# Kernel tuning notes

Measured on AMD Instinct MI355X. Metric: run time of the kernel, lower is better.

## Reference

```python
import jax, jax.numpy as jnp
import numpy as np

N = 100000   # nodes
E = 1600000  # edges (avg degree 16)
IN, HID, OUT, HEADS = 8, 32, 16, 4


def setup_inputs() -> dict:
    key = jax.random.key(0)
    ks = jax.random.split(key, 12)
    def g(k, shape, fan):
        return (jax.random.normal(k, shape, jnp.float32) / np.float32(np.sqrt(fan)))
    x = jax.random.normal(ks[0], (N, IN), jnp.float32)
    edge_index = jax.random.randint(ks[1], (2, E), 0, N, dtype=jnp.int64)
    return {
        "x": x,
        "edge_index": edge_index,
        "W1": g(ks[2], (IN, HEADS * HID), IN),
        "att_src1": g(ks[3], (HEADS, HID), HID),
        "att_dst1": g(ks[4], (HEADS, HID), HID),
        "b1": jnp.zeros((HEADS * HID,), jnp.float32),
        "W2": g(ks[5], (HEADS * HID, OUT), HEADS * HID),
        "att_src2": g(ks[6], (1, OUT), OUT),
        "att_dst2": g(ks[7], (1, OUT), OUT),
        "b2": jnp.zeros((OUT,), jnp.float32),
        "Wc1": g(ks[8], (OUT, 8), OUT),
        "bc1": jnp.zeros((8,), jnp.float32),
        "Wc2": g(ks[9], (8, 1), 8),
        "bc2": jnp.zeros((1,), jnp.float32),
    }


def _gat_layer(x, W, att_src, att_dst, bias, src, dst, n, concat):
    """PyG GATConv (eval mode): gather -> per-edge attention -> segment softmax -> scatter."""
    H, D = att_src.shape
    h = (x @ W).reshape(n, H, D)                       # [N,H,D]
    a_s = jnp.einsum("nhd,hd->nh", h, att_src)          # [N,H]
    a_d = jnp.einsum("nhd,hd->nh", h, att_dst)          # [N,H]
    e = jax.nn.leaky_relu(a_s[src] + a_d[dst], 0.2)     # [Etot,H]
    m = jax.ops.segment_max(e, dst, num_segments=n)     # per-dst max for stable softmax
    m = jnp.where(jnp.isfinite(m), m, 0.0)
    e = jnp.exp(e - m[dst])
    denom = jax.ops.segment_sum(e, dst, num_segments=n)
    alpha = e / (denom[dst] + 1e-16)                    # [Etot,H]
    out = jax.ops.segment_sum(h[src] * alpha[:, :, None], dst, num_segments=n)  # [N,H,D]
    out = out.reshape(n, H * D) if concat else out.mean(axis=1)
    return out + bias


def reference(x, edge_index, W1, att_src1, att_dst1, b1, W2, att_src2, att_dst2, b2, Wc1, bc1, Wc2, bc2):
    n = x.shape[0]
    loops = jnp.arange(n, dtype=edge_index.dtype)       # add_self_loops=True (PyG default)
    src = jnp.concatenate([edge_index[0], loops])
    dst = jnp.concatenate([edge_index[1], loops])
    h = jax.nn.elu(_gat_layer(x, W1, att_src1, att_dst1, b1, src, dst, n, concat=True))
    emb = jax.nn.elu(_gat_layer(h, W2, att_src2, att_dst2, b2, src, dst, n, concat=False))
    risk = jax.nn.sigmoid(jax.nn.relu(emb @ Wc1 + bc1) @ Wc2 + bc2)
    return emb, risk
```

## Files before the change

kernel.cpp:

```cpp
#include <hip/hip_runtime.h>
#include <hip/hip_fp16.h>
#include <math.h>

#define N_NODES 100000
#define N_EDGES 1600000
#define F_IN 8
#define HID 32
#define HEADS 4
#define F1 128
#define F2 16
#define NB 391
#define NBLK_BIN 391
#define NBLK_A 391
#define BCAP 4864

__device__ __forceinline__ float leaky(float x){ return x > 0.f ? x : 0.2f * x; }
__device__ __forceinline__ float elu1(float x){ return x > 0.f ? x : __expf(x) - 1.f; }

__global__ __launch_bounds__(256) void k_bin_attn(
    const int* __restrict__ src, const int* __restrict__ dst,
    int* __restrict__ bucketCnt, unsigned int* __restrict__ ebuf,
    const float* __restrict__ x, const float* __restrict__ W1,
    const float* __restrict__ as1w, const float* __restrict__ ad1w,
    float* __restrict__ xa){
    __shared__ float smem[1344];
    int t = threadIdx.x;
    if (blockIdx.x < NBLK_BIN){
        int* hist    = (int*)smem;
        int* basePos = hist + NB;
        int* cur     = basePos + NB;
        for (int j = t; j < NB; j += 256) hist[j] = 0;
        __syncthreads();
        int base = blockIdx.x * 4096;
        int dv[16];
        #pragma unroll
        for (int j = 0; j < 16; j++){
            int e = base + j * 256 + t;
            dv[j] = (e < N_EDGES) ? dst[e] : -1;
            if (dv[j] >= 0) atomicAdd(&hist[dv[j] >> 8], 1);
        }
        __syncthreads();
        for (int j = t; j < NB; j += 256){
            int h = hist[j];
            if (h) basePos[j] = atomicAdd(&bucketCnt[j], h);
            cur[j] = 0;
        }
        __syncthreads();
        #pragma unroll
        for (int j = 0; j < 16; j++){
            if (dv[j] >= 0){
                int e = base + j * 256 + t;
                int d = dv[j];
                int b = d >> 8;
                int off = atomicAdd(&cur[b], 1);
                ebuf[b * BCAP + basePos[b] + off] = ((unsigned)(d & 255) << 17) | (unsigned)src[e];
            }
        }
    } else {
        float* W1s  = smem;
        float* atts = smem + 1024;
        float* attd = smem + 1152;
        float* cs   = smem + 1280;
        float* cd   = smem + 1312;
        ((float4*)W1s)[t] = ((const float4*)W1)[t];
        if (t < 128){ atts[t] = as1w[t]; attd[t] = ad1w[t]; }
        __syncthreads();
        if (t < 64){
            int m = t & 7, h = (t >> 3) & 3;
            bool sel = t >= 32;
            const float* wrow = W1s + m * F1 + h * 32;
            const float* av   = (sel ? attd : atts) + h * 32;
            float s = 0.f;
            #pragma unroll
            for (int d = 0; d < 32; d++) s += wrow[d] * av[d];
            (sel ? cd : cs)[h * 8 + m] = s;
        }
        __syncthreads();
        int n = (blockIdx.x - NBLK_BIN) * 256 + t;
        if (n < N_NODES){
            float4 x0 = ((const float4*)x)[n * 2];
            float4 x1 = ((const float4*)x)[n * 2 + 1];
            float4 osv, odv;
            float* po = (float*)&osv;
            float* pd = (float*)&odv;
            #pragma unroll
            for (int h = 0; h < 4; h++){
                const float* c0 = cs + h * 8;
                const float* c1 = cd + h * 8;
                po[h] = x0.x*c0[0] + x0.y*c0[1] + x0.z*c0[2] + x0.w*c0[3]
                      + x1.x*c0[4] + x1.y*c0[5] + x1.z*c0[6] + x1.w*c0[7];
                pd[h] = x0.x*c1[0] + x0.y*c1[1] + x0.z*c1[2] + x0.w*c1[3]
                      + x1.x*c1[4] + x1.y*c1[5] + x1.z*c1[6] + x1.w*c1[7];
            }
            float* px = xa + (size_t)n * 16;
            *(float4*)(px)      = x0;
            *(float4*)(px + 4)  = x1;
            *(float4*)(px + 8)  = osv;
            *(float4*)(px + 12) = odv;
        }
    }
}

__global__ __launch_bounds__(256) void k_local_csr(
    const int* __restrict__ bucketCnt, const unsigned int* __restrict__ ebuf,
    int* __restrict__ row_ptr, int* __restrict__ esrc){
    __shared__ int deg[256];
    __shared__ int scn[256];
    __shared__ int cntAll[NB];
    __shared__ unsigned int segs[BCAP];
    int b = blockIdx.x, t = threadIdx.x;
    deg[t] = 0;
    for (int j = t; j < NB; j += 256) cntAll[j] = bucketCnt[j];
    __syncthreads();
    int partial = 0;
    for (int j = t; j < b; j += 256) partial += cntAll[j];
    scn[t] = partial;
    __syncthreads();
    for (int off = 128; off > 0; off >>= 1){
        if (t < off) scn[t] += scn[t + off];
        __syncthreads();
    }
    int sbase = scn[0];
    int cnt = cntAll[b];
    __syncthreads();
    const unsigned int* seg = ebuf + b * BCAP;
    for (int i = t; i < cnt; i += 256){
        unsigned int e = seg[i];
        segs[i] = e;
        atomicAdd(&deg[e >> 17], 1);
    }
    __syncthreads();
    int v = deg[t];
    scn[t] = v;
    __syncthreads();
    for (int off = 1; off < 256; off <<= 1){
        int xx = (t >= off) ? scn[t - off] : 0;
        __syncthreads();
        scn[t] += xx;
        __syncthreads();
    }
    int excl = scn[t] - v;
    int start = sbase + excl;
    int n = b * 256 + t;
    if (n < N_NODES) row_ptr[n] = start;
    if (b == NB - 1 && t == 0) row_ptr[N_NODES] = sbase + cnt;
    deg[t] = start;
    __syncthreads();
    for (int i = t; i < cnt; i += 256){
        unsigned int e = segs[i];
        int pos = atomicAdd(&deg[e >> 17], 1);
        esrc[pos] = (int)(e & 0x1FFFFu);
    }
}

__global__ __launch_bounds__(256) void k_agg1(
    const float* __restrict__ xa, const int* __restrict__ row_ptr, const int* __restrict__ esrc,
    float* __restrict__ xagg, float* __restrict__ dden){
    int t = threadIdx.x;
    int wv = t >> 6, lane = t & 63;
    int n = blockIdx.x * 4 + wv;
    int g = lane >> 4;
    int l = lane & 15;
    int hd = l >> 2;
    int c2 = (l & 3) * 2;

    float vn = xa[(size_t)n * 16 + l];
    float adh = __shfl(vn, 12 + hd, 16);

    float den = 0.f, ac0 = 0.f, ac1 = 0.f;
    if (g == 0){
        float w = __expf(leaky(__shfl(vn, 8 + hd, 16) + adh));
        den = w;
        ac0 = w * __shfl(vn, c2, 16);
        ac1 = w * __shfl(vn, c2 + 1, 16);
    }
    int start = row_ptr[n], end = row_ptr[n + 1];
    int len = end - start;
    int chunk = (len + 3) >> 2;
    int i = start + g * chunk;
    int e = i + chunk; if (e > end) e = end;
    for (; i + 3 < e; i += 4){
        int s0 = esrc[i], s1 = esrc[i + 1], s2 = esrc[i + 2], s3 = esrc[i + 3];
        float v0 = xa[(size_t)s0 * 16 + l];
        float v1 = xa[(size_t)s1 * 16 + l];
        float v2 = xa[(size_t)s2 * 16 + l];
        float v3 = xa[(size_t)s3 * 16 + l];
        float w0 = __expf(leaky(__shfl(v0, 8 + hd, 16) + adh));
        float w1 = __expf(leaky(__shfl(v1, 8 + hd, 16) + adh));
        float w2 = __expf(leaky(__shfl(v2, 8 + hd, 16) + adh));
        float w3 = __expf(leaky(__shfl(v3, 8 + hd, 16) + adh));
        den += (w0 + w1) + (w2 + w3);
        ac0 = fmaf(w0, __shfl(v0, c2, 16), ac0); ac1 = fmaf(w0, __shfl(v0, c2 + 1, 16), ac1);
        ac0 = fmaf(w1, __shfl(v1, c2, 16), ac0); ac1 = fmaf(w1, __shfl(v1, c2 + 1, 16), ac1);
        ac0 = fmaf(w2, __shfl(v2, c2, 16), ac0); ac1 = fmaf(w2, __shfl(v2, c2 + 1, 16), ac1);
        ac0 = fmaf(w3, __shfl(v3, c2, 16), ac0); ac1 = fmaf(w3, __shfl(v3, c2 + 1, 16), ac1);
    }
    for (; i < e; i++){
        int s0 = esrc[i];
        float v0 = xa[(size_t)s0 * 16 + l];
        float w0 = __expf(leaky(__shfl(v0, 8 + hd, 16) + adh));
        den += w0;
        ac0 = fmaf(w0, __shfl(v0, c2, 16), ac0); ac1 = fmaf(w0, __shfl(v0, c2 + 1, 16), ac1);
    }
    den += __shfl_xor(den, 16); den += __shfl_xor(den, 32);
    ac0 += __shfl_xor(ac0, 16); ac0 += __shfl_xor(ac0, 32);
    ac1 += __shfl_xor(ac1, 16); ac1 += __shfl_xor(ac1, 32);

    if (lane < 16){
        float2 o; o.x = ac0; o.y = ac1;
        *(float2*)(xagg + (size_t)n * 32 + 2 * l) = o;
        if ((l & 3) == 0) dden[(size_t)n * 4 + hd] = den;
    }
}

__global__ __launch_bounds__(256) void k_epi(
    const float* __restrict__ xagg, const float* __restrict__ dden,
    const float* __restrict__ W1, const float* __restrict__ W2,
    const float* __restrict__ b1, const float* __restrict__ as2w, const float* __restrict__ ad2w,
    __half* __restrict__ h2h, float* __restrict__ a_s2, float* __restrict__ a_d2){
    __shared__ __half2 W1h[F_IN * 64];
    __shared__ __half2 W2t[F2 * 64];
    __shared__ __half2 hlsh[16 * 68];
    int t = threadIdx.x;
    {
        float4 w1v = ((const float4*)W1)[t];
        int m = t >> 5, j = (2 * t) & 63;
        W1h[m * 64 + j]     = __floats2half2_rn(w1v.x, w1v.y);
        W1h[m * 64 + j + 1] = __floats2half2_rn(w1v.z, w1v.w);
        #pragma unroll
        for (int hf = 0; hf < 2; hf++){
            int p = t + hf * 256;
            float4 wv = ((const float4*)W2)[p];
            int k = p >> 2, dbase = (p & 3) * 4;
            float vals[4] = {wv.x, wv.y, wv.z, wv.w};
            #pragma unroll
            for (int c = 0; c < 4; c++){
                int dw = (dbase + c) * 64 + (k >> 1);
                int sdw = dw ^ (((dw >> 6) & 7) << 2);
                ((__half*)W2t)[2 * sdw + (k & 1)] = __float2half(vals[c]);
            }
        }
    }
    __syncthreads();

    int nn = t >> 4, q = t & 15;
    int n = blockIdx.x * 16 + nn;
    int hd = q >> 2;

    const float* xg = xagg + (size_t)n * 32 + hd * 8;
    float4 xga = *(const float4*)(xg);
    float4 xgb = *(const float4*)(xg + 4);
    float invd = 1.f / dden[(size_t)n * 4 + hd];
    float xv[8] = {xga.x, xga.y, xga.z, xga.w, xgb.x, xgb.y, xgb.z, xgb.w};
    float pre[8] = {0,0,0,0,0,0,0,0};
    #pragma unroll
    for (int m = 0; m < 8; m++){
        float4 raw = *(const float4*)(W1h + m * 64 + 4 * q);
        const __half2* wp = (const __half2*)&raw;
        float xm = xv[m];
        float2 f0 = __half22float2(wp[0]);
        float2 f1 = __half22float2(wp[1]);
        float2 f2 = __half22float2(wp[2]);
        float2 f3 = __half22float2(wp[3]);
        pre[0] = fmaf(xm, f0.x, pre[0]); pre[1] = fmaf(xm, f0.y, pre[1]);
        pre[2] = fmaf(xm, f1.x, pre[2]); pre[3] = fmaf(xm, f1.y, pre[3]);
        pre[4] = fmaf(xm, f2.x, pre[4]); pre[5] = fmaf(xm, f2.y, pre[5]);
        pre[6] = fmaf(xm, f3.x, pre[6]); pre[7] = fmaf(xm, f3.y, pre[7]);
    }
    float4 ba = *(const float4*)(b1 + 8 * q);
    float4 bb = *(const float4*)(b1 + 8 * q + 4);
    __half2 hout[4];
    hout[0] = __floats2half2_rn(elu1(pre[0] * invd + ba.x), elu1(pre[1] * invd + ba.y));
    hout[1] = __floats2half2_rn(elu1(pre[2] * invd + ba.z), elu1(pre[3] * invd + ba.w));
    hout[2] = __floats2half2_rn(elu1(pre[4] * invd + bb.x), elu1(pre[5] * invd + bb.y));
    hout[3] = __floats2half2_rn(elu1(pre[6] * invd + bb.z), elu1(pre[7] * invd + bb.w));
    *(float4*)(hlsh + nn * 68 + 4 * q) = *(float4*)hout;
    __syncthreads();

    float dot = 0.f;
    #pragma unroll
    for (int ob = 0; ob < 8; ob++){
        __half2 acc2 = __float2half2_rn(0.f);
        #pragma unroll
        for (int kb = ob * 2; kb < ob * 2 + 2; kb++){
            float4 hr = *(const float4*)(hlsh + nn * 68 + 4 * kb);
            int dwb = 64 * q + 4 * kb;
            float4 wr = *(const float4*)(W2t + (dwb ^ (((dwb >> 6) & 7) << 2)));
            const __half2* hp  = (const __half2*)&hr;
            const __half2* wp2 = (const __half2*)&wr;
            acc2 = __hfma2(hp[0], wp2[0], acc2);
            acc2 = __hfma2(hp[1], wp2[1], acc2);
            acc2 = __hfma2(hp[2], wp2[2], acc2);
            acc2 = __hfma2(hp[3], wp2[3], acc2);
        }
        float2 fa = __half22float2(acc2);
        dot += fa.x + fa.y;
    }
    float ps = dot * as2w[q];
    float pd = dot * ad2w[q];
    #pragma unroll
    for (int off = 8; off >= 1; off >>= 1){
        ps += __shfl_down(ps, off, 16);
        pd += __shfl_down(pd, off, 16);
    }
    if (q == 0){ a_s2[n] = ps; a_d2[n] = pd; }
    h2h[(size_t)n * F2 + q] = __float2half(dot);
}

__global__ __launch_bounds__(256) void k_agg2(
    const __half* __restrict__ h2h, const float* __restrict__ a_s2, const float* __restrict__ a_d2,
    const int* __restrict__ row_ptr, const int* __restrict__ esrc,
    const float* __restrict__ b2, const float* __restrict__ Wc1, const float* __restrict__ bc1,
    const float* __restrict__ Wc2, const float* __restrict__ bc2, float* __restrict__ out){
    int t = threadIdx.x;
    int wv = t >> 6, lane = t & 63;
    int n = blockIdx.x * 4 + wv;
    int g = lane >> 3;
    int l = lane & 7;
    float adn = a_d2[n];
    const __half* hb2 = h2h + 2 * l;

    float den = 0.f, acc0 = 0.f, acc1 = 0.f;
    if (g == 0){
        float w = __expf(leaky(a_s2[n] + adn));
        den = w;
        float2 f = __half22float2(*(const __half2*)(hb2 + ((unsigned)n << 4)));
        acc0 = w * f.x; acc1 = w * f.y;
    }
    int start = row_ptr[n], end = row_ptr[n + 1];
    int len = end - start;
    int chunk = (len + 7) >> 3;
    int i = start + g * chunk;
    int e = i + chunk; if (e > end) e = end;
    for (int base = i; base < e; base += 4){
        bool v1 = base + 1 < e, v2 = base + 2 < e, v3 = base + 3 < e;
        int s0 = esrc[base];
        int s1 = v1 ? esrc[base + 1] : s0;
        int s2 = v2 ? esrc[base + 2] : s0;
        int s3 = v3 ? esrc[base + 3] : s0;
        float a0 = a_s2[s0], a1 = a_s2[s1], a2 = a_s2[s2], a3 = a_s2[s3];
        __half2 p0 = *(const __half2*)(hb2 + ((unsigned)s0 << 4));
        __half2 p1 = *(const __half2*)(hb2 + ((unsigned)s1 << 4));
        __half2 p2 = *(const __half2*)(hb2 + ((unsigned)s2 << 4));
        __half2 p3 = *(const __half2*)(hb2 + ((unsigned)s3 << 4));
        float w0 = __expf(leaky(a0 + adn));
        float w1 = v1 ? __expf(leaky(a1 + adn)) : 0.f;
        float w2 = v2 ? __expf(leaky(a2 + adn)) : 0.f;
        float w3 = v3 ? __expf(leaky(a3 + adn)) : 0.f;
        den += (w0 + w1) + (w2 + w3);
        float2 f0 = __half22float2(p0), f1 = __half22float2(p1);
        float2 f2 = __half22float2(p2), f3 = __half22float2(p3);
        acc0 += w0 * f0.x + w1 * f1.x + w2 * f2.x + w3 * f3.x;
        acc1 += w0 * f0.y + w1 * f1.y + w2 * f2.y + w3 * f3.y;
    }
    #pragma unroll
    for (int off = 8; off <= 32; off <<= 1){
        den  += __shfl_xor(den, off);
        acc0 += __shfl_xor(acc0, off);
        acc1 += __shfl_xor(acc1, off);
    }
    float inv = 1.f / (den + 1e-16f);
    float e0v = elu1(acc0 * inv + b2[2 * l]);
    float e1v = elu1(acc1 * inv + b2[2 * l + 1]);
    if (g == 0){
        float2 ov; ov.x = e0v; ov.y = e1v;
        *(float2*)(out + (size_t)n * 16 + 2 * l) = ov;
    }
    float hid = bc1[l];
    #pragma unroll
    for (int j = 0; j < 8; j++){
        float a = __shfl(e0v, j, 8);
        float b = __shfl(e1v, j, 8);
        hid += a * Wc1[(2 * j) * 8 + l] + b * Wc1[(2 * j + 1) * 8 + l];
    }
    float contrib = fmaxf(hid, 0.f) * Wc2[l];
    contrib += __shfl_xor(contrib, 1);
    contrib += __shfl_xor(contrib, 2);
    contrib += __shfl_xor(contrib, 4);
    if (lane == 0) out[(size_t)N_NODES * 16 + n] = 1.f / (1.f + __expf(-(contrib + bc2[0])));
}

extern "C" void kernel_launch(void* const* d_in, const int* in_sizes, int n_in,
                              void* d_out, int out_size, void* d_ws, size_t ws_size,
                              hipStream_t stream){
    const float* x    = (const float*)d_in[0];
    const int*   ei   = (const int*)d_in[1];
    const float* W1   = (const float*)d_in[2];
    const float* as1w = (const float*)d_in[3];
    const float* ad1w = (const float*)d_in[4];
    const float* b1   = (const float*)d_in[5];
    const float* W2   = (const float*)d_in[6];
    const float* as2w = (const float*)d_in[7];
    const float* ad2w = (const float*)d_in[8];
    const float* b2   = (const float*)d_in[9];
    const float* Wc1  = (const float*)d_in[10];
    const float* bc1  = (const float*)d_in[11];
    const float* Wc2  = (const float*)d_in[12];
    const float* bc2  = (const float*)d_in[13];
    float* out = (float*)d_out;
    const int* src = ei;
    const int* dst = ei + N_EDGES;

    float* ws   = (float*)d_ws;
    float* a_s2 = ws;
    float* a_d2 = a_s2 + N_NODES;
    float* xa   = a_d2 + N_NODES;
    float* xagg = xa + (size_t)N_NODES * 16;
    float* dden = xagg + (size_t)N_NODES * 32;
    __half* h2h = (__half*)(dden + (size_t)N_NODES * 4);
    int* bucketCnt = (int*)(h2h + (size_t)N_NODES * 16);
    int* row_ptr  = bucketCnt + NB;
    int* esrc     = row_ptr + N_NODES + 1;
    unsigned int* ebuf = (unsigned int*)(esrc + N_EDGES);

    hipMemsetAsync(bucketCnt, 0, NB * sizeof(int), stream);
    k_bin_attn<<<NBLK_BIN + NBLK_A, 256, 0, stream>>>(
        src, dst, bucketCnt, ebuf, x, W1, as1w, ad1w, xa);
    k_local_csr<<<NB, 256, 0, stream>>>(bucketCnt, ebuf, row_ptr, esrc);
    k_agg1<<<N_NODES / 4, 256, 0, stream>>>(xa, row_ptr, esrc, xagg, dden);
    k_epi<<<N_NODES / 16, 256, 0, stream>>>(
        xagg, dden, W1, W2, b1, as2w, ad2w, h2h, a_s2, a_d2);
    k_agg2<<<N_NODES / 4, 256, 0, stream>>>(h2h, a_s2, a_d2, row_ptr, esrc, b2, Wc1, bc1, Wc2, bc2, out);
}
```

Measured before the change: 242.1 us.

## Halve edges per bin block, widen CSR blocks, predicate agg1 tail loop

The binning kernel now handles 2048 edges per block over twice as many blocks. The local CSR kernel runs with 512 threads per block, and only the first 256 threads do the per-node scan. The agg1 gather loop drops its scalar remainder loop in favour of a predicated 4-wide body that zeroes out-of-range weights. The aim is more parallelism in the preprocessing stages and better memory-level parallelism on short edge tails, at the cost of extra global atomics on bucket counts and some redundant loads.

```diff
diff --git a/kernel.cpp b/kernel.cpp
--- a/kernel.cpp
+++ b/kernel.cpp
@@ -10,7 +10,8 @@
 #define F1 128
 #define F2 16
 #define NB 391
-#define NBLK_BIN 391
+#define NBLK_BIN 782
+#define EDGES_PER_BIN 2048
 #define NBLK_A 391
 #define BCAP 4864
 
@@ -31,10 +32,10 @@
         int* cur     = basePos + NB;
         for (int j = t; j < NB; j += 256) hist[j] = 0;
         __syncthreads();
-        int base = blockIdx.x * 4096;
-        int dv[16];
+        int base = blockIdx.x * EDGES_PER_BIN;
+        int dv[8];
         #pragma unroll
-        for (int j = 0; j < 16; j++){
+        for (int j = 0; j < 8; j++){
             int e = base + j * 256 + t;
             dv[j] = (e < N_EDGES) ? dst[e] : -1;
             if (dv[j] >= 0) atomicAdd(&hist[dv[j] >> 8], 1);
@@ -47,7 +48,7 @@
         }
         __syncthreads();
         #pragma unroll
-        for (int j = 0; j < 16; j++){
+        for (int j = 0; j < 8; j++){
             if (dv[j] >= 0){
                 int e = base + j * 256 + t;
                 int d = dv[j];
@@ -101,22 +102,22 @@
     }
 }
 
-__global__ __launch_bounds__(256) void k_local_csr(
+__global__ __launch_bounds__(512) void k_local_csr(
     const int* __restrict__ bucketCnt, const unsigned int* __restrict__ ebuf,
     int* __restrict__ row_ptr, int* __restrict__ esrc){
     __shared__ int deg[256];
-    __shared__ int scn[256];
+    __shared__ int scn[512];
     __shared__ int cntAll[NB];
     __shared__ unsigned int segs[BCAP];
     int b = blockIdx.x, t = threadIdx.x;
-    deg[t] = 0;
-    for (int j = t; j < NB; j += 256) cntAll[j] = bucketCnt[j];
+    if (t < 256) deg[t] = 0;
+    for (int j = t; j < NB; j += 512) cntAll[j] = bucketCnt[j];
     __syncthreads();
     int partial = 0;
-    for (int j = t; j < b; j += 256) partial += cntAll[j];
+    for (int j = t; j < b; j += 512) partial += cntAll[j];
     scn[t] = partial;
     __syncthreads();
-    for (int off = 128; off > 0; off >>= 1){
+    for (int off = 256; off > 0; off >>= 1){
         if (t < off) scn[t] += scn[t + off];
         __syncthreads();
     }
@@ -124,29 +125,31 @@
     int cnt = cntAll[b];
     __syncthreads();
     const unsigned int* seg = ebuf + b * BCAP;
-    for (int i = t; i < cnt; i += 256){
+    for (int i = t; i < cnt; i += 512){
         unsigned int e = seg[i];
         segs[i] = e;
         atomicAdd(&deg[e >> 17], 1);
     }
     __syncthreads();
-    int v = deg[t];
-    scn[t] = v;
+    int v = (t < 256) ? deg[t] : 0;
+    if (t < 256) scn[t] = v;
     __syncthreads();
     for (int off = 1; off < 256; off <<= 1){
-        int xx = (t >= off) ? scn[t - off] : 0;
-        __syncthreads();
-        scn[t] += xx;
-        __syncthreads();
-    }
-    int excl = scn[t] - v;
-    int start = sbase + excl;
-    int n = b * 256 + t;
-    if (n < N_NODES) row_ptr[n] = start;
+        int xx = (t < 256 && t >= off) ? scn[t - off] : 0;
+        __syncthreads();
+        if (t < 256) scn[t] += xx;
+        __syncthreads();
+    }
+    if (t < 256){
+        int excl = scn[t] - v;
+        int start = sbase + excl;
+        int n = b * 256 + t;
+        if (n < N_NODES) row_ptr[n] = start;
+        deg[t] = start;
+    }
     if (b == NB - 1 && t == 0) row_ptr[N_NODES] = sbase + cnt;
-    deg[t] = start;
-    __syncthreads();
-    for (int i = t; i < cnt; i += 256){
+    __syncthreads();
+    for (int i = t; i < cnt; i += 512){
         unsigned int e = segs[i];
         int pos = atomicAdd(&deg[e >> 17], 1);
         esrc[pos] = (int)(e & 0x1FFFFu);
@@ -179,28 +182,25 @@
     int chunk = (len + 3) >> 2;
     int i = start + g * chunk;
     int e = i + chunk; if (e > end) e = end;
-    for (; i + 3 < e; i += 4){
-        int s0 = esrc[i], s1 = esrc[i + 1], s2 = esrc[i + 2], s3 = esrc[i + 3];
+    for (int base = i; base < e; base += 4){
+        bool b1v = base + 1 < e, b2v = base + 2 < e, b3v = base + 3 < e;
+        int s0 = esrc[base];
+        int s1 = b1v ? esrc[base + 1] : s0;
+        int s2 = b2v ? esrc[base + 2] : s0;
+        int s3 = b3v ? esrc[base + 3] : s0;
         float v0 = xa[(size_t)s0 * 16 + l];
         float v1 = xa[(size_t)s1 * 16 + l];
         float v2 = xa[(size_t)s2 * 16 + l];
         float v3 = xa[(size_t)s3 * 16 + l];
         float w0 = __expf(leaky(__shfl(v0, 8 + hd, 16) + adh));
-        float w1 = __expf(leaky(__shfl(v1, 8 + hd, 16) + adh));
-        float w2 = __expf(leaky(__shfl(v2, 8 + hd, 16) + adh));
-        float w3 = __expf(leaky(__shfl(v3, 8 + hd, 16) + adh));
+        float w1 = b1v ? __expf(leaky(__shfl(v1, 8 + hd, 16) + adh)) : 0.f;
+        float w2 = b2v ? __expf(leaky(__shfl(v2, 8 + hd, 16) + adh)) : 0.f;
+        float w3 = b3v ? __expf(leaky(__shfl(v3, 8 + hd, 16) + adh)) : 0.f;
         den += (w0 + w1) + (w2 + w3);
         ac0 = fmaf(w0, __shfl(v0, c2, 16), ac0); ac1 = fmaf(w0, __shfl(v0, c2 + 1, 16), ac1);
         ac0 = fmaf(w1, __shfl(v1, c2, 16), ac0); ac1 = fmaf(w1, __shfl(v1, c2 + 1, 16), ac1);
         ac0 = fmaf(w2, __shfl(v2, c2, 16), ac0); ac1 = fmaf(w2, __shfl(v2, c2 + 1, 16), ac1);
         ac0 = fmaf(w3, __shfl(v3, c2, 16), ac0); ac1 = fmaf(w3, __shfl(v3, c2 + 1, 16), ac1);
-    }
-    for (; i < e; i++){
-        int s0 = esrc[i];
-        float v0 = xa[(size_t)s0 * 16 + l];
-        float w0 = __expf(leaky(__shfl(v0, 8 + hd, 16) + adh));
-        den += w0;
-        ac0 = fmaf(w0, __shfl(v0, c2, 16), ac0); ac1 = fmaf(w0, __shfl(v0, c2 + 1, 16), ac1);
     }
     den += __shfl_xor(den, 16); den += __shfl_xor(den, 32);
     ac0 += __shfl_xor(ac0, 16); ac0 += __shfl_xor(ac0, 32);
@@ -416,7 +416,7 @@
     hipMemsetAsync(bucketCnt, 0, NB * sizeof(int), stream);
     k_bin_attn<<<NBLK_BIN + NBLK_A, 256, 0, stream>>>(
         src, dst, bucketCnt, ebuf, x, W1, as1w, ad1w, xa);
-    k_local_csr<<<NB, 256, 0, stream>>>(bucketCnt, ebuf, row_ptr, esrc);
+    k_local_csr<<<NB, 512, 0, stream>>>(bucketCnt, ebuf, row_ptr, esrc);
     k_agg1<<<N_NODES / 4, 256, 0, stream>>>(xa, row_ptr, esrc, xagg, dden);
     k_epi<<<N_NODES / 16, 256, 0, stream>>>(
         xagg, dden, W1, W2, b1, as2w, ad2w, h2h, a_s2, a_d2);
```

Result: no change. 243.2 us (+0.5%).
